# Performance work log

Measured on AMD Instinct MI355X. Metric: run time of the kernel, lower is better.

The kernel has to match this reference:

```python
import jax, jax.numpy as jnp
import numpy as np

N, K, D = 32768, 32, 64
LOG_2PI = float(np.log(2.0 * np.pi))


def setup_inputs() -> dict:
    key = jax.random.key(0)
    k1, k2, k3, k4 = jax.random.split(key, 4)
    X = jax.random.normal(k1, (N, D), dtype=jnp.float32)
    mu = jax.random.normal(k2, (K, D), dtype=jnp.float32)
    L = jax.random.normal(k3, (K, D, D), dtype=jnp.float32) * 0.1
    weights = jax.random.normal(k4, (K,), dtype=jnp.float32)
    return {"X": X, "mu": mu, "L": L, "weights": weights, "it": 0}


def reference(X, mu, L, weights, it):
    d = X.shape[1]
    # Cholesky composition: Sigma_k = tril(L_k) @ tril(L_k).T + I  (always PD)
    Lt = jnp.tril(L)                                   # [K, D, D]
    sigmas = Lt @ jnp.swapaxes(Lt, -1, -2) + jnp.eye(d, dtype=X.dtype)
    _, logdet = jnp.linalg.slogdet(sigmas)             # [K] (det > 0, sign = +1)
    Sinv = jnp.linalg.inv(sigmas)                      # [K, D, D]
    # Batched squared Mahalanobis distance: [N, K]
    diff = X[:, None, :] - mu[None, :, :]              # [N, K, D]
    maha = jnp.einsum("nkd,kde,nke->nk", diff, Sinv, diff)
    log_w = jax.nn.log_softmax(weights)                # [K]
    # log component density + log mixture weight
    logp = -0.5 * (d * LOG_2PI + logdet[None, :] + maha) + log_w[None, :]
    # pdf = sum_k exp(logp); log_likelihood = log(pdf)  (stable via logsumexp)
    loglik = jax.scipy.special.logsumexp(logp, axis=1)  # [N]
    # forward = -log_likelihoods(X).logsumexp(dim=0)
    return -jax.scipy.special.logsumexp(loglik, axis=0)
```

## Files before the change

### kernel.cpp

```cpp
#include <hip/hip_runtime.h>
#include <math.h>

#define DIM 64
#define KC 32
#define NPTS 32768
#define LOG_2PI 1.8378770664093453f
#define C0 (-58.0f)
#define ST 68

typedef __attribute__((ext_vector_type(8))) short short8;
typedef __attribute__((ext_vector_type(4))) float float4v;

__device__ __forceinline__ unsigned short f2bf(float f) {
    unsigned u = __float_as_uint(f);
    u += 0x7FFFu + ((u >> 16) & 1u);
    return (unsigned short)(u >> 16);
}

__device__ __forceinline__ float rdlane(float v, int l) {
    return __int_as_float(__builtin_amdgcn_readlane(__float_as_int(v), l));
}

template <int CTRL>
__device__ __forceinline__ float dpp_add(float x) {
    int t = __builtin_amdgcn_mov_dpp(__float_as_int(x), CTRL, 0xF, 0xF, true);
    return x + __int_as_float(t);
}
__device__ __forceinline__ float sum16(float x) {
    x = dpp_add<0xB1>(x);
    x = dpp_add<0x4E>(x);
    x = dpp_add<0x141>(x);
    x = dpp_add<0x140>(x);
    return x;
}

__global__ __launch_bounds__(256) void prep_kernel(
    const float* __restrict__ L, const float* __restrict__ mu,
    const float* __restrict__ w, short* __restrict__ Bpack,
    float* __restrict__ cstC)
{
    const int k = blockIdx.x;
    const int t = threadIdx.x;
    const int wv = t >> 6;
    const int ln = t & 63;
    __shared__ float Llds[DIM * ST];
    __shared__ float Sig[DIM * ST];
    __shared__ float Clds[DIM * ST];
    __shared__ float Ylds[DIM * ST];
    __shared__ float qlds[DIM];
    __shared__ float rdbuf[DIM];
    __shared__ float ldet;

    for (int idx = t; idx < DIM * DIM; idx += 256) {
        int r = idx >> 6, c = idx & 63;
        float v = L[(size_t)k * DIM * DIM + idx];
        Llds[r * ST + c] = (c <= r) ? v : 0.f;
    }
    for (int idx = t; idx < DIM * ST; idx += 256) {
        Clds[idx] = 0.f;
        Ylds[idx] = 0.f;
    }
    __syncthreads();

    {
        float Lr[DIM];
        const float2* lp = (const float2*)(Llds + ln * ST);
#pragma unroll
        for (int p = 0; p < 32; ++p) {
            float2 v = lp[p];
            Lr[2 * p] = v.x; Lr[2 * p + 1] = v.y;
        }
#pragma unroll 1
        for (int jj = 0; jj < 16; ++jj) {
            const int j = wv * 16 + jj;
            const float2* up = (const float2*)(Llds + j * ST);
            float a0 = 0.f, a1 = 0.f, a2 = 0.f, a3 = 0.f;
#pragma unroll
            for (int p = 0; p < 32; p += 2) {
                float2 u0 = up[p], u1 = up[p + 1];
                a0 = fmaf(Lr[2 * p], u0.x, a0);
                a1 = fmaf(Lr[2 * p + 1], u0.y, a1);
                a2 = fmaf(Lr[2 * p + 2], u1.x, a2);
                a3 = fmaf(Lr[2 * p + 3], u1.y, a3);
            }
            float s = (a0 + a1) + (a2 + a3);
            if (j == ln) s += 1.f;
            Sig[ln * ST + j] = s;
        }
    }
    __syncthreads();

    {
        const float2* crow = (const float2*)(Clds + ln * ST);
        const float2* yrow = (const float2*)(Ylds + ln * ST);
        float ld2 = 0.f;
#pragma unroll 1
        for (int c = 0; c < DIM; c += 4) {
            const float2* u0 = (const float2*)(Clds + (c + 0) * ST);
            const float2* u1 = (const float2*)(Clds + (c + 1) * ST);
            const float2* u2 = (const float2*)(Clds + (c + 2) * ST);
            const float2* u3 = (const float2*)(Clds + (c + 3) * ST);
            float si0 = 0.f, si1 = 0.f, si2 = 0.f, si3 = 0.f;
            if (wv == 0) {
                float d0a = 0.f, d0b = 0.f, d1a = 0.f, d1b = 0.f;
                float d2a = 0.f, d2b = 0.f, d3a = 0.f, d3b = 0.f;
#pragma unroll
                for (int p = 0; p < 32; ++p) {
                    float2 cr = crow[p];
                    float2 a0 = u0[p], a1 = u1[p], a2 = u2[p], a3 = u3[p];
                    d0a = fmaf(cr.x, a0.x, d0a); d0b = fmaf(cr.y, a0.y, d0b);
                    d1a = fmaf(cr.x, a1.x, d1a); d1b = fmaf(cr.y, a1.y, d1b);
                    d2a = fmaf(cr.x, a2.x, d2a); d2b = fmaf(cr.y, a2.y, d2b);
                    d3a = fmaf(cr.x, a3.x, d3a); d3b = fmaf(cr.y, a3.y, d3b);
                }
                const float4 sg = *(const float4*)(Sig + ln * ST + c);
                float s0 = sg.x - (d0a + d0b);
                float s1 = sg.y - (d1a + d1b);
                float s2 = sg.z - (d2a + d2b);
                float s3 = sg.w - (d3a + d3b);
                float dd0 = rdlane(s0, c + 0);
                float rd0 = __builtin_amdgcn_rsqf(dd0);
                float c0v = s0 * rd0;
                s1 = fmaf(-c0v, rdlane(c0v, c + 1), s1);
                s2 = fmaf(-c0v, rdlane(c0v, c + 2), s2);
                s3 = fmaf(-c0v, rdlane(c0v, c + 3), s3);
                float dd1 = rdlane(s1, c + 1);
                float rd1 = __builtin_amdgcn_rsqf(dd1);
                float c1v = s1 * rd1;
                s2 = fmaf(-c1v, rdlane(c1v, c + 2), s2);
                s3 = fmaf(-c1v, rdlane(c1v, c + 3), s3);
                float dd2 = rdlane(s2, c + 2);
                float rd2 = __builtin_amdgcn_rsqf(dd2);
                float c2v = s2 * rd2;
                s3 = fmaf(-c2v, rdlane(c2v, c + 3), s3);
                float dd3 = rdlane(s3, c + 3);
                float rd3 = __builtin_amdgcn_rsqf(dd3);
                float c3v = s3 * rd3;
                ld2 += (__logf(dd0) + __logf(dd1)) + (__logf(dd2) + __logf(dd3));
                *(float4*)(Clds + ln * ST + c) = make_float4(c0v, c1v, c2v, c3v);
                if (ln == 0) *(float4*)(rdbuf + c) = make_float4(rd0, rd1, rd2, rd3);
            } else if (wv == 1) {
                float e0a = 0.f, e0b = 0.f, e1a = 0.f, e1b = 0.f;
                float e2a = 0.f, e2b = 0.f, e3a = 0.f, e3b = 0.f;
#pragma unroll
                for (int p = 0; p < 32; ++p) {
                    float2 yr = yrow[p];
                    float2 a0 = u0[p], a1 = u1[p], a2 = u2[p], a3 = u3[p];
                    e0a = fmaf(yr.x, a0.x, e0a); e0b = fmaf(yr.y, a0.y, e0b);
                    e1a = fmaf(yr.x, a1.x, e1a); e1b = fmaf(yr.y, a1.y, e1b);
                    e2a = fmaf(yr.x, a2.x, e2a); e2b = fmaf(yr.y, a2.y, e2b);
                    e3a = fmaf(yr.x, a3.x, e3a); e3b = fmaf(yr.y, a3.y, e3b);
                }
                si0 = ((ln == c + 0) ? 1.f : 0.f) - (e0a + e0b);
                si1 = ((ln == c + 1) ? 1.f : 0.f) - (e1a + e1b);
                si2 = ((ln == c + 2) ? 1.f : 0.f) - (e2a + e2b);
                si3 = ((ln == c + 3) ? 1.f : 0.f) - (e3a + e3b);
            }
            __syncthreads();
            if (wv == 1) {
                const float4 rdv = *(const float4*)(rdbuf + c);
                float C10 = Clds[(c + 1) * ST + c];
                float C20 = Clds[(c + 2) * ST + c];
                float C21 = Clds[(c + 2) * ST + c + 1];
                float C30 = Clds[(c + 3) * ST + c];
                float C31 = Clds[(c + 3) * ST + c + 1];
                float C32 = Clds[(c + 3) * ST + c + 2];
                float y0 = si0 * rdv.x;
                float y1 = (si1 - C10 * y0) * rdv.y;
                float y2 = (si2 - C20 * y0 - C21 * y1) * rdv.z;
                float y3 = (si3 - C30 * y0 - C31 * y1 - C32 * y2) * rdv.w;
                float4 yo;
                yo.x = (ln <= c + 0) ? y0 : 0.f;
                yo.y = (ln <= c + 1) ? y1 : 0.f;
                yo.z = (ln <= c + 2) ? y2 : 0.f;
                yo.w = (ln <= c + 3) ? y3 : 0.f;
                *(float4*)(Ylds + ln * ST + c) = yo;
            }
        }
        if (wv == 0 && ln == 0) ldet = ld2;
    }
    __syncthreads();

    if (wv == 0) {
        const float* muk = mu + k * DIM;
        float qv = 0.f;
#pragma unroll 8
        for (int j = 0; j < DIM; ++j)
            qv = fmaf(Ylds[j * ST + ln], muk[j], qv);
        qlds[ln] = qv;
        if (ln == 0) {
            float wm = -3.0e38f;
            for (int i = 0; i < KC; ++i) wm = fmaxf(wm, w[i]);
            float se = 0.f;
            for (int i = 0; i < KC; ++i) se += __expf(w[i] - wm);
            float logw = w[k] - (wm + __logf(se));
            cstC[k] = -0.5f * (DIM * LOG_2PI + ldet) + logw - C0;
        }
    }
    __syncthreads();

    {
        const int ct = wv;
        const int col = ct * 16 + (ln & 15);
        const int kb = (ln >> 4) * 8;
#pragma unroll
        for (int kt = 0; kt < 3; ++kt) {
            short8 v;
            if (kt < 2) {
#pragma unroll
                for (int e = 0; e < 8; ++e)
                    v[e] = (short)f2bf(Ylds[(kt * 32 + kb + e) * ST + col]);
            } else {
#pragma unroll
                for (int e = 0; e < 8; ++e)
                    v[e] = (short)((kb + e == 0) ? f2bf(-qlds[col]) : 0);
            }
            *(short8*)(Bpack + ((size_t)(k * 12 + ct * 3 + kt) * 64 + ln) * 8) = v;
        }
    }
}

__global__ __launch_bounds__(256, 2) void main_kernel(
    const float* __restrict__ X, const float* __restrict__ Bpack,
    const float* __restrict__ cstC, float* __restrict__ partials)
{
    const int tid = threadIdx.x;
    const int lane = tid & 63;
    const int wv = tid >> 6;
    const int ks = blockIdx.x & 7;
    const int g = blockIdx.x >> 3;

    __shared__ float4 Bsh[3072];
    {
        const float4* Bg = (const float4*)Bpack + (size_t)ks * 3072;
#pragma unroll
        for (int it = 0; it < 12; ++it)
            Bsh[it * 256 + tid] = Bg[it * 256 + tid];
    }

    const int rbase = g * 128 + wv * 32;
    const int jb = (lane >> 4) * 8;
    const float* Xr0 = X + (size_t)(rbase + (lane & 15)) * DIM;
    const float* Xr1 = Xr0 + 16 * DIM;
    short8 a0, a1, b0r, b1r;
#pragma unroll
    for (int e = 0; e < 8; ++e) {
        a0[e] = (short)f2bf(Xr0[jb + e]);
        a1[e] = (short)f2bf(Xr0[32 + jb + e]);
        b0r[e] = (short)f2bf(Xr1[jb + e]);
        b1r[e] = (short)f2bf(Xr1[32 + jb + e]);
    }
    short8 a2 = (short8)0;
    if (lane < 16) a2[0] = (short)0x3F80;

    __syncthreads();

    const short8* Bs = (const short8*)Bsh;
    float acc = 0.f;
#pragma unroll
    for (int kk = 0; kk < 4; ++kk) {
        const int k = ks * 4 + kk;
        float p0 = 0.f, p1 = 0.f, p2 = 0.f, p3 = 0.f;
        float r0 = 0.f, r1 = 0.f, r2 = 0.f, r3 = 0.f;
#pragma unroll
        for (int ct = 0; ct < 4; ++ct) {
            short8 f0 = Bs[(kk * 12 + ct * 3 + 0) * 64 + lane];
            short8 f1 = Bs[(kk * 12 + ct * 3 + 1) * 64 + lane];
            short8 f2 = Bs[(kk * 12 + ct * 3 + 2) * 64 + lane];
            float4v c0 = {0.f, 0.f, 0.f, 0.f};
            c0 = __builtin_amdgcn_mfma_f32_16x16x32_bf16(a0, f0, c0, 0, 0, 0);
            c0 = __builtin_amdgcn_mfma_f32_16x16x32_bf16(a1, f1, c0, 0, 0, 0);
            c0 = __builtin_amdgcn_mfma_f32_16x16x32_bf16(a2, f2, c0, 0, 0, 0);
            float4v c1 = {0.f, 0.f, 0.f, 0.f};
            c1 = __builtin_amdgcn_mfma_f32_16x16x32_bf16(b0r, f0, c1, 0, 0, 0);
            c1 = __builtin_amdgcn_mfma_f32_16x16x32_bf16(b1r, f1, c1, 0, 0, 0);
            c1 = __builtin_amdgcn_mfma_f32_16x16x32_bf16(a2, f2, c1, 0, 0, 0);
            p0 = fmaf(c0[0], c0[0], p0); p1 = fmaf(c0[1], c0[1], p1);
            p2 = fmaf(c0[2], c0[2], p2); p3 = fmaf(c0[3], c0[3], p3);
            r0 = fmaf(c1[0], c1[0], r0); r1 = fmaf(c1[1], c1[1], r1);
            r2 = fmaf(c1[2], c1[2], r2); r3 = fmaf(c1[3], c1[3], r3);
        }
        const float cc = cstC[k];
        acc += __expf(fmaf(-0.5f, sum16(p0), cc)) + __expf(fmaf(-0.5f, sum16(p1), cc));
        acc += __expf(fmaf(-0.5f, sum16(p2), cc)) + __expf(fmaf(-0.5f, sum16(p3), cc));
        acc += __expf(fmaf(-0.5f, sum16(r0), cc)) + __expf(fmaf(-0.5f, sum16(r1), cc));
        acc += __expf(fmaf(-0.5f, sum16(r2), cc)) + __expf(fmaf(-0.5f, sum16(r3), cc));
    }
    acc += __shfl_xor(acc, 16, 64);
    acc += __shfl_xor(acc, 32, 64);

    __shared__ float pm[4];
    if (lane == 0) pm[wv] = acc;
    __syncthreads();
    if (tid == 0)
        partials[blockIdx.x] = (pm[0] + pm[1]) + (pm[2] + pm[3]);
}

__global__ __launch_bounds__(256) void final_kernel(
    const float* __restrict__ partials, int n, float* __restrict__ out)
{
    const int tid = threadIdx.x;
    float s = 0.f;
    for (int i = tid; i < n; i += 256) s += partials[i];
#pragma unroll
    for (int m = 1; m <= 32; m <<= 1) s += __shfl_xor(s, m, 64);
    __shared__ float pm[4];
    if ((tid & 63) == 0) pm[tid >> 6] = s;
    __syncthreads();
    if (tid == 0) out[0] = -(C0 + logf((pm[0] + pm[1]) + (pm[2] + pm[3])));
}

extern "C" void kernel_launch(void* const* d_in, const int* in_sizes, int n_in,
                              void* d_out, int out_size, void* d_ws, size_t ws_size,
                              hipStream_t stream) {
    const float* X  = (const float*)d_in[0];
    const float* mu = (const float*)d_in[1];
    const float* L  = (const float*)d_in[2];
    const float* w  = (const float*)d_in[3];

    char* ws = (char*)d_ws;
    short* Bpack = (short*)ws;
    float* cstC  = (float*)(ws + 32 * 12 * 64 * 8 * 2);
    float* parts = cstC + KC;

    prep_kernel<<<KC, 256, 0, stream>>>(L, mu, w, Bpack, cstC);
    main_kernel<<<2048, 256, 0, stream>>>(X, (const float*)Bpack, cstC, parts);
    final_kernel<<<1, 256, 0, stream>>>(parts, 2048, (float*)d_out);
}
```

Baseline: 113.2 us.

## Pre-convert X to bf16 in prep kernel and skip zero blocks in triangular products

Extra blocks in the prep kernel convert X to bf16 once, running in parallel with the per-component Cholesky work. The main kernel, which reads X once per component-slice block (8x in total), now loads half as many bytes as vector loads and no longer converts. The prep kernel's L·Lᵀ and Cholesky/inverse inner products also stop at the triangular bound using float4 LDS reads, skipping the known-zero upper parts. The cost is an extra bf16 copy of X written to and read back from workspace.

```diff
diff --git a/kernel.cpp b/kernel.cpp
--- a/kernel.cpp
+++ b/kernel.cpp
@@ -7,6 +7,7 @@
 #define LOG_2PI 1.8378770664093453f
 #define C0 (-58.0f)
 #define ST 68
+#define CONVBLK 1024
 
 typedef __attribute__((ext_vector_type(8))) short short8;
 typedef __attribute__((ext_vector_type(4))) float float4v;
@@ -35,10 +36,24 @@
 }
 
 __global__ __launch_bounds__(256) void prep_kernel(
-    const float* __restrict__ L, const float* __restrict__ mu,
-    const float* __restrict__ w, short* __restrict__ Bpack,
-    float* __restrict__ cstC)
+    const float* __restrict__ X, const float* __restrict__ L,
+    const float* __restrict__ mu, const float* __restrict__ w,
+    short* __restrict__ Bpack, float* __restrict__ cstC,
+    short* __restrict__ Xbf)
 {
+    if (blockIdx.x >= KC) {
+        const int ctid = (blockIdx.x - KC) * 256 + threadIdx.x;
+        const float4* xin = (const float4*)X + (size_t)ctid * 2;
+        float4 v0 = xin[0], v1 = xin[1];
+        short8 o;
+        o[0] = (short)f2bf(v0.x); o[1] = (short)f2bf(v0.y);
+        o[2] = (short)f2bf(v0.z); o[3] = (short)f2bf(v0.w);
+        o[4] = (short)f2bf(v1.x); o[5] = (short)f2bf(v1.y);
+        o[6] = (short)f2bf(v1.z); o[7] = (short)f2bf(v1.w);
+        *((short8*)Xbf + ctid) = o;
+        return;
+    }
+
     const int k = blockIdx.x;
     const int t = threadIdx.x;
     const int wv = t >> 6;
@@ -72,16 +87,17 @@
         }
 #pragma unroll 1
         for (int jj = 0; jj < 16; ++jj) {
-            const int j = wv * 16 + jj;
-            const float2* up = (const float2*)(Llds + j * ST);
+            const int j = jj * 4 + wv;
+            const float4* up = (const float4*)(Llds + j * ST);
+            const int pc = (j >> 2) + 1;
             float a0 = 0.f, a1 = 0.f, a2 = 0.f, a3 = 0.f;
-#pragma unroll
-            for (int p = 0; p < 32; p += 2) {
-                float2 u0 = up[p], u1 = up[p + 1];
-                a0 = fmaf(Lr[2 * p], u0.x, a0);
-                a1 = fmaf(Lr[2 * p + 1], u0.y, a1);
-                a2 = fmaf(Lr[2 * p + 2], u1.x, a2);
-                a3 = fmaf(Lr[2 * p + 3], u1.y, a3);
+#pragma unroll 4
+            for (int p = 0; p < pc; ++p) {
+                float4 u = up[p];
+                a0 = fmaf(Lr[4 * p], u.x, a0);
+                a1 = fmaf(Lr[4 * p + 1], u.y, a1);
+                a2 = fmaf(Lr[4 * p + 2], u.z, a2);
+                a3 = fmaf(Lr[4 * p + 3], u.w, a3);
             }
             float s = (a0 + a1) + (a2 + a3);
             if (j == ln) s += 1.f;
@@ -91,27 +107,32 @@
     __syncthreads();
 
     {
-        const float2* crow = (const float2*)(Clds + ln * ST);
-        const float2* yrow = (const float2*)(Ylds + ln * ST);
+        const float4* crow = (const float4*)(Clds + ln * ST);
+        const float4* yrow = (const float4*)(Ylds + ln * ST);
         float ld2 = 0.f;
 #pragma unroll 1
         for (int c = 0; c < DIM; c += 4) {
-            const float2* u0 = (const float2*)(Clds + (c + 0) * ST);
-            const float2* u1 = (const float2*)(Clds + (c + 1) * ST);
-            const float2* u2 = (const float2*)(Clds + (c + 2) * ST);
-            const float2* u3 = (const float2*)(Clds + (c + 3) * ST);
+            const float4* u0 = (const float4*)(Clds + (c + 0) * ST);
+            const float4* u1 = (const float4*)(Clds + (c + 1) * ST);
+            const float4* u2 = (const float4*)(Clds + (c + 2) * ST);
+            const float4* u3 = (const float4*)(Clds + (c + 3) * ST);
+            const int pc = (c >> 2) + 1;
             float si0 = 0.f, si1 = 0.f, si2 = 0.f, si3 = 0.f;
             if (wv == 0) {
                 float d0a = 0.f, d0b = 0.f, d1a = 0.f, d1b = 0.f;
                 float d2a = 0.f, d2b = 0.f, d3a = 0.f, d3b = 0.f;
-#pragma unroll
-                for (int p = 0; p < 32; ++p) {
-                    float2 cr = crow[p];
-                    float2 a0 = u0[p], a1 = u1[p], a2 = u2[p], a3 = u3[p];
+#pragma unroll 4
+                for (int p = 0; p < pc; ++p) {
+                    float4 cr = crow[p];
+                    float4 a0 = u0[p], a1 = u1[p], a2 = u2[p], a3 = u3[p];
                     d0a = fmaf(cr.x, a0.x, d0a); d0b = fmaf(cr.y, a0.y, d0b);
+                    d0a = fmaf(cr.z, a0.z, d0a); d0b = fmaf(cr.w, a0.w, d0b);
                     d1a = fmaf(cr.x, a1.x, d1a); d1b = fmaf(cr.y, a1.y, d1b);
+                    d1a = fmaf(cr.z, a1.z, d1a); d1b = fmaf(cr.w, a1.w, d1b);
                     d2a = fmaf(cr.x, a2.x, d2a); d2b = fmaf(cr.y, a2.y, d2b);
+                    d2a = fmaf(cr.z, a2.z, d2a); d2b = fmaf(cr.w, a2.w, d2b);
                     d3a = fmaf(cr.x, a3.x, d3a); d3b = fmaf(cr.y, a3.y, d3b);
+                    d3a = fmaf(cr.z, a3.z, d3a); d3b = fmaf(cr.w, a3.w, d3b);
                 }
                 const float4 sg = *(const float4*)(Sig + ln * ST + c);
                 float s0 = sg.x - (d0a + d0b);
@@ -142,14 +163,18 @@
             } else if (wv == 1) {
                 float e0a = 0.f, e0b = 0.f, e1a = 0.f, e1b = 0.f;
                 float e2a = 0.f, e2b = 0.f, e3a = 0.f, e3b = 0.f;
-#pragma unroll
-                for (int p = 0; p < 32; ++p) {
-                    float2 yr = yrow[p];
-                    float2 a0 = u0[p], a1 = u1[p], a2 = u2[p], a3 = u3[p];
+#pragma unroll 4
+                for (int p = 0; p < pc; ++p) {
+                    float4 yr = yrow[p];
+                    float4 a0 = u0[p], a1 = u1[p], a2 = u2[p], a3 = u3[p];
                     e0a = fmaf(yr.x, a0.x, e0a); e0b = fmaf(yr.y, a0.y, e0b);
+                    e0a = fmaf(yr.z, a0.z, e0a); e0b = fmaf(yr.w, a0.w, e0b);
                     e1a = fmaf(yr.x, a1.x, e1a); e1b = fmaf(yr.y, a1.y, e1b);
+                    e1a = fmaf(yr.z, a1.z, e1a); e1b = fmaf(yr.w, a1.w, e1b);
                     e2a = fmaf(yr.x, a2.x, e2a); e2b = fmaf(yr.y, a2.y, e2b);
+                    e2a = fmaf(yr.z, a2.z, e2a); e2b = fmaf(yr.w, a2.w, e2b);
                     e3a = fmaf(yr.x, a3.x, e3a); e3b = fmaf(yr.y, a3.y, e3b);
+                    e3a = fmaf(yr.z, a3.z, e3a); e3b = fmaf(yr.w, a3.w, e3b);
                 }
                 si0 = ((ln == c + 0) ? 1.f : 0.f) - (e0a + e0b);
                 si1 = ((ln == c + 1) ? 1.f : 0.f) - (e1a + e1b);
@@ -221,7 +246,7 @@
 }
 
 __global__ __launch_bounds__(256, 2) void main_kernel(
-    const float* __restrict__ X, const float* __restrict__ Bpack,
+    const short* __restrict__ Xbf, const float* __restrict__ Bpack,
     const float* __restrict__ cstC, float* __restrict__ partials)
 {
     const int tid = threadIdx.x;
@@ -240,16 +265,12 @@
 
     const int rbase = g * 128 + wv * 32;
     const int jb = (lane >> 4) * 8;
-    const float* Xr0 = X + (size_t)(rbase + (lane & 15)) * DIM;
-    const float* Xr1 = Xr0 + 16 * DIM;
-    short8 a0, a1, b0r, b1r;
-#pragma unroll
-    for (int e = 0; e < 8; ++e) {
-        a0[e] = (short)f2bf(Xr0[jb + e]);
-        a1[e] = (short)f2bf(Xr0[32 + jb + e]);
-        b0r[e] = (short)f2bf(Xr1[jb + e]);
-        b1r[e] = (short)f2bf(Xr1[32 + jb + e]);
-    }
+    const int j8 = jb >> 3;
+    const short8* xr = (const short8*)Xbf + (size_t)(rbase + (lane & 15)) * 8;
+    short8 a0  = xr[j8];
+    short8 a1  = xr[j8 + 4];
+    short8 b0r = xr[j8 + 128];
+    short8 b1r = xr[j8 + 132];
     short8 a2 = (short8)0;
     if (lane < 16) a2[0] = (short)0x3F80;
 
@@ -322,8 +343,9 @@
     short* Bpack = (short*)ws;
     float* cstC  = (float*)(ws + 32 * 12 * 64 * 8 * 2);
     float* parts = cstC + KC;
-
-    prep_kernel<<<KC, 256, 0, stream>>>(L, mu, w, Bpack, cstC);
-    main_kernel<<<2048, 256, 0, stream>>>(X, (const float*)Bpack, cstC, parts);
+    short* Xbf   = (short*)(ws + (4 << 20));
+
+    prep_kernel<<<KC + CONVBLK, 256, 0, stream>>>(X, L, mu, w, Bpack, cstC, Xbf);
+    main_kernel<<<2048, 256, 0, stream>>>(Xbf, (const float*)Bpack, cstC, parts);
     final_kernel<<<1, 256, 0, stream>>>(parts, 2048, (float*)d_out);
 }
```

Result: slower. 122.8 us (+8.5%).
